# Kernel tuning notes

Measured on AMD Instinct MI355X. Metric: run time of the kernel, lower is better.

The kernel has to match this reference:

```python
import jax, jax.numpy as jnp
import numpy as np

N, A, C = 2048, 256, 100   # batch, feat_dim, num_classes
LAT = A // 2               # latent_dim = feat_dim // 2
BN_EPS = 1e-5


def setup_inputs() -> dict:
    key = jax.random.key(0)
    ks = jax.random.split(key, 8)
    s = jax.random.normal(ks[0], (N, A), dtype=jnp.float32)
    y = jax.random.randint(ks[1], (N,), 0, C)
    ratio = jnp.float32(0.5)
    W1 = jax.random.normal(ks[2], (LAT, A), dtype=jnp.float32) / np.sqrt(A)
    b1 = jnp.zeros((LAT,), jnp.float32)
    gamma = jnp.ones((LAT,), jnp.float32)
    beta = jnp.zeros((LAT,), jnp.float32)
    W2 = jax.random.normal(ks[3], (A, LAT), dtype=jnp.float32) / np.sqrt(LAT)
    b2 = jnp.zeros((A,), jnp.float32)
    Wfc = jax.random.normal(ks[4], (C, A), dtype=jnp.float32) / np.sqrt(A)
    bfc = jnp.zeros((C,), jnp.float32)
    # per-class covariance table [C, A, A], symmetric PSD like a real EstimatorCV state
    M = jax.random.normal(ks[5], (C, A, A), dtype=jnp.float32)
    cov = jnp.einsum('cab,cdb->cad', M, M) / A
    return {"s": s, "y": y, "ratio": ratio, "W1": W1, "b1": b1,
            "gamma": gamma, "beta": beta, "W2": W2, "b2": b2,
            "Wfc": Wfc, "bfc": bfc, "cov": cov}


def reference(s, y, ratio, W1, b1, gamma, beta, W2, b2, Wfc, bfc, cov):
    # pred: Linear -> BatchNorm1d (train-mode batch stats) -> ReLU -> Linear -> ReLU
    h = s @ W1.T + b1                                   # [N, LAT]
    mu = jnp.mean(h, axis=0)
    var = jnp.var(h, axis=0)                            # biased, as torch BN
    h = (h - mu) / jnp.sqrt(var + BN_EPS) * gamma + beta
    h = jax.nn.relu(h)
    f = jax.nn.relu(h @ W2.T + b2)                      # [N, A]
    z = f @ Wfc.T + bfc                                 # [N, C]

    # correct_z: diag of (W_i - W_y) cov[y] (W_i - W_y)^T, computed without the
    # wasted off-diagonal bmm of the original
    cov_sg = jax.lax.stop_gradient(cov)                 # cov is detached in source
    Wy = Wfc[y]                                         # [N, A]
    diff = Wfc[None, :, :] - Wy[:, None, :]             # [N, C, A]
    CVy = cov_sg[y]                                     # [N, A, A]
    tmp = jnp.einsum('nca,nab->ncb', diff, CVy)         # [N, C, A]
    sigma2 = jnp.sum(tmp * diff, axis=-1)               # [N, C] = diag of quad form
    return z + ratio * 0.5 * sigma2
```

## Files before the change

### kernel.cpp

```cpp
#include <hip/hip_runtime.h>

#define Nn  2048
#define Aa  256
#define Cc  100
#define LAT 128
#define BN_EPS 1e-5f

#define OFF_HB   0
#define OFF_SUMS (OFF_HB + Nn*LAT/2)
#define OFF_SP   (OFF_SUMS + 128*256)

typedef __attribute__((ext_vector_type(8))) short bf16x8;
typedef __attribute__((ext_vector_type(4))) float f32x4;

__device__ __forceinline__ short f2bf(float f) {
    unsigned u = __float_as_uint(f);
    u = (u + 0x7FFFu + ((u >> 16) & 1u)) >> 16;
    return (short)u;
}
__device__ __forceinline__ float bf2f(short h) {
    return __uint_as_float(((unsigned)(unsigned short)h) << 16);
}

#define DPITCH 264

__global__ __launch_bounds__(256) void kA(
    const float* __restrict__ s, const float* __restrict__ W1,
    const float* __restrict__ b1, const float* __restrict__ Wfc,
    const float* __restrict__ cov,
    short* __restrict__ hB, float* __restrict__ sums, float* __restrict__ Spart)
{
    __shared__ __align__(16) char smem[112 * DPITCH * 2 + 4 * 112 * 4];
    const int bid = blockIdx.x;
    const int t = threadIdx.x;
    const int w = t >> 6, l = t & 63, il = l & 15, q = l >> 4;

    if (bid < 200) {
        short* Dlds = (short*)smem;
        float (*red)[112] = (float(*)[112])(smem + 112 * DPITCH * 2);
        const int k  = bid >> 1;
        const int nh = bid & 1;
        const float* covk = cov + (size_t)k * (Aa * Aa);

        {
            const int c4 = t & 63;
            float4 wk = *(const float4*)&Wfc[(size_t)k * Aa + c4 * 4];
#pragma unroll
            for (int j = 0; j < 28; j++) {
                int row = (t >> 6) + j * 4;
                short4 o;
                if (row < Cc) {
                    float4 v = *(const float4*)&Wfc[(size_t)row * Aa + c4 * 4];
                    o.x = f2bf(v.x - wk.x); o.y = f2bf(v.y - wk.y);
                    o.z = f2bf(v.z - wk.z); o.w = f2bf(v.w - wk.w);
                } else {
                    o.x = 0; o.y = 0; o.z = 0; o.w = 0;
                }
                *(short4*)&Dlds[row * DPITCH + c4 * 4] = o;
            }
        }
        __syncthreads();

        const int bbase = nh * 128 + w * 32;

        f32x4 acc[7][2];
#pragma unroll
        for (int m = 0; m < 7; m++) {
            acc[m][0] = (f32x4){0.f,0.f,0.f,0.f};
            acc[m][1] = (f32x4){0.f,0.f,0.f,0.f};
        }

        const float* brow0 = covk + (size_t)(bbase + il) * Aa;
        const float* brow1 = covk + (size_t)(bbase + 16 + il) * Aa;

#pragma unroll
        for (int sgk = 0; sgk < 8; sgk++) {
            const int a0 = sgk * 32 + q * 8;
            bf16x8 bm0, bm1;
            {
                float4 u0 = *(const float4*)&brow0[a0];
                float4 u1 = *(const float4*)&brow0[a0 + 4];
                bm0[0]=f2bf(u0.x); bm0[1]=f2bf(u0.y); bm0[2]=f2bf(u0.z); bm0[3]=f2bf(u0.w);
                bm0[4]=f2bf(u1.x); bm0[5]=f2bf(u1.y); bm0[6]=f2bf(u1.z); bm0[7]=f2bf(u1.w);
                float4 v0 = *(const float4*)&brow1[a0];
                float4 v1 = *(const float4*)&brow1[a0 + 4];
                bm1[0]=f2bf(v0.x); bm1[1]=f2bf(v0.y); bm1[2]=f2bf(v0.z); bm1[3]=f2bf(v0.w);
                bm1[4]=f2bf(v1.x); bm1[5]=f2bf(v1.y); bm1[6]=f2bf(v1.z); bm1[7]=f2bf(v1.w);
            }
#pragma unroll
            for (int m = 0; m < 7; m++) {
                bf16x8 am = *(bf16x8*)&Dlds[(m * 16 + il) * DPITCH + a0];
                acc[m][0] = __builtin_amdgcn_mfma_f32_16x16x32_bf16(am, bm0, acc[m][0], 0, 0, 0);
                acc[m][1] = __builtin_amdgcn_mfma_f32_16x16x32_bf16(am, bm1, acc[m][1], 0, 0, 0);
            }
        }

#pragma unroll
        for (int m = 0; m < 7; m++) {
            float sacc[4] = {0.f, 0.f, 0.f, 0.f};
#pragma unroll
            for (int nf = 0; nf < 2; nf++) {
                int bcol = bbase + nf * 16 + il;
#pragma unroll
                for (int r = 0; r < 4; r++) {
                    int crow = m * 16 + q * 4 + r;
                    float dv = bf2f(Dlds[crow * DPITCH + bcol]);
                    sacc[r] = fmaf(dv, acc[m][nf][r], sacc[r]);
                }
            }
#pragma unroll
            for (int r = 0; r < 4; r++) {
                float v = sacc[r];
                v += __shfl_xor(v, 1);
                v += __shfl_xor(v, 2);
                v += __shfl_xor(v, 4);
                v += __shfl_xor(v, 8);
                if (il == 0) red[w][m * 16 + q * 4 + r] = v;
            }
        }
        __syncthreads();
        if (t < Cc)
            Spart[nh * (Cc * Cc) + k * Cc + t] =
                red[0][t] + red[1][t] + red[2][t] + red[3][t];
    } else {
        const int bid2 = bid - 200;
        const int row0 = bid2 * 16;
        const int colw = w * 32;

        f32x4 acc[2];
        acc[0] = (f32x4){0.f,0.f,0.f,0.f};
        acc[1] = (f32x4){0.f,0.f,0.f,0.f};

        const float* arow = s  + (size_t)(row0 + il) * Aa;
        const float* bp0  = W1 + (size_t)(colw + il) * Aa;
        const float* bp1  = W1 + (size_t)(colw + 16 + il) * Aa;

#pragma unroll
        for (int ks = 0; ks < 8; ks++) {
            const int k0 = ks * 32 + q * 8;
            float4 u0 = *(const float4*)&arow[k0];
            float4 u1 = *(const float4*)&arow[k0 + 4];
            bf16x8 am;
            am[0]=f2bf(u0.x); am[1]=f2bf(u0.y); am[2]=f2bf(u0.z); am[3]=f2bf(u0.w);
            am[4]=f2bf(u1.x); am[5]=f2bf(u1.y); am[6]=f2bf(u1.z); am[7]=f2bf(u1.w);
            float4 v0 = *(const float4*)&bp0[k0];
            float4 v1 = *(const float4*)&bp0[k0 + 4];
            bf16x8 bm0;
            bm0[0]=f2bf(v0.x); bm0[1]=f2bf(v0.y); bm0[2]=f2bf(v0.z); bm0[3]=f2bf(v0.w);
            bm0[4]=f2bf(v1.x); bm0[5]=f2bf(v1.y); bm0[6]=f2bf(v1.z); bm0[7]=f2bf(v1.w);
            float4 x0 = *(const float4*)&bp1[k0];
            float4 x1 = *(const float4*)&bp1[k0 + 4];
            bf16x8 bm1;
            bm1[0]=f2bf(x0.x); bm1[1]=f2bf(x0.y); bm1[2]=f2bf(x0.z); bm1[3]=f2bf(x0.w);
            bm1[4]=f2bf(x1.x); bm1[5]=f2bf(x1.y); bm1[6]=f2bf(x1.z); bm1[7]=f2bf(x1.w);
            acc[0] = __builtin_amdgcn_mfma_f32_16x16x32_bf16(am, bm0, acc[0], 0, 0, 0);
            acc[1] = __builtin_amdgcn_mfma_f32_16x16x32_bf16(am, bm1, acc[1], 0, 0, 0);
        }

#pragma unroll
        for (int n = 0; n < 2; n++) {
            const int col = colw + n * 16 + il;
            const float bias = b1[col];
            float s1 = 0.f, s2 = 0.f;
#pragma unroll
            for (int r = 0; r < 4; r++) {
                float v = acc[n][r] + bias;
                hB[(size_t)(row0 + q * 4 + r) * LAT + col] = f2bf(v);
                s1 += v; s2 += v * v;
            }
            s1 += __shfl_xor(s1, 16); s1 += __shfl_xor(s1, 32);
            s2 += __shfl_xor(s2, 16); s2 += __shfl_xor(s2, 32);
            if (q == 0) {
                sums[bid2 * 256 + col]       = s1;
                sums[bid2 * 256 + 128 + col] = s2;
            }
        }
    }
}

#define FPITCH 264

__global__ __launch_bounds__(256) void kB(
    const short* __restrict__ hB, const float* __restrict__ sums,
    const float* __restrict__ gamma, const float* __restrict__ beta,
    const float* __restrict__ W2, const float* __restrict__ b2,
    const float* __restrict__ Wfc, const float* __restrict__ bfc,
    const float* __restrict__ Spart, const int* __restrict__ y,
    const float* __restrict__ ratio, float* __restrict__ out)
{
    __shared__ float scL[LAT], shL[LAT];
    __shared__ short fLDS[16 * FPITCH];
    const int t = threadIdx.x;
    const int w = t >> 6, l = t & 63, il = l & 15, q = l >> 4;
    const int row0 = blockIdx.x * 16;

    if (t < 128) {
        float a1 = 0.f, a2 = 0.f;
#pragma unroll 8
        for (int b = 0; b < 128; b++) {
            a1 += sums[b * 256 + t];
            a2 += sums[b * 256 + 128 + t];
        }
        float mu  = a1 * (1.0f / Nn);
        float var = a2 * (1.0f / Nn) - mu * mu;
        float inv = rsqrtf(var + BN_EPS);
        float sc  = gamma[t] * inv;
        scL[t] = sc;
        shL[t] = beta[t] - mu * sc;
    }
    __syncthreads();

    f32x4 acc3[4];
#pragma unroll
    for (int n = 0; n < 4; n++) acc3[n] = (f32x4){0.f,0.f,0.f,0.f};

    const short* arow = hB + (size_t)(row0 + il) * LAT;
#pragma unroll
    for (int ks = 0; ks < 4; ks++) {
        const int k0 = ks * 32 + q * 8;
        bf16x8 ha = *(const bf16x8*)&arow[k0];
        bf16x8 am;
#pragma unroll
        for (int j = 0; j < 8; j++) {
            float fv = fmaf(bf2f(ha[j]), scL[k0 + j], shL[k0 + j]);
            am[j] = f2bf(fmaxf(fv, 0.f));
        }
#pragma unroll
        for (int n = 0; n < 4; n++) {
            const int col = w * 64 + n * 16 + il;
            float4 v0 = *(const float4*)&W2[(size_t)col * LAT + k0];
            float4 v1 = *(const float4*)&W2[(size_t)col * LAT + k0 + 4];
            bf16x8 bm;
            bm[0]=f2bf(v0.x); bm[1]=f2bf(v0.y); bm[2]=f2bf(v0.z); bm[3]=f2bf(v0.w);
            bm[4]=f2bf(v1.x); bm[5]=f2bf(v1.y); bm[6]=f2bf(v1.z); bm[7]=f2bf(v1.w);
            acc3[n] = __builtin_amdgcn_mfma_f32_16x16x32_bf16(am, bm, acc3[n], 0, 0, 0);
        }
    }
#pragma unroll
    for (int n = 0; n < 4; n++) {
        const int col = w * 64 + n * 16 + il;
        const float bias = b2[col];
#pragma unroll
        for (int r = 0; r < 4; r++) {
            float v = fmaxf(acc3[n][r] + bias, 0.f);
            fLDS[(q * 4 + r) * FPITCH + col] = f2bf(v);
        }
    }
    __syncthreads();

    f32x4 acc4[2];
    acc4[0] = (f32x4){0.f,0.f,0.f,0.f};
    acc4[1] = (f32x4){0.f,0.f,0.f,0.f};
#pragma unroll
    for (int ks = 0; ks < 8; ks++) {
        const int k0 = ks * 32 + q * 8;
        bf16x8 am = *(const bf16x8*)&fLDS[il * FPITCH + k0];
#pragma unroll
        for (int n = 0; n < 2; n++) {
            const int col = w * 32 + n * 16 + il;
            const int crow = col < Cc ? col : Cc - 1;
            float4 v0 = *(const float4*)&Wfc[(size_t)crow * Aa + k0];
            float4 v1 = *(const float4*)&Wfc[(size_t)crow * Aa + k0 + 4];
            bf16x8 bm;
            bm[0]=f2bf(v0.x); bm[1]=f2bf(v0.y); bm[2]=f2bf(v0.z); bm[3]=f2bf(v0.w);
            bm[4]=f2bf(v1.x); bm[5]=f2bf(v1.y); bm[6]=f2bf(v1.z); bm[7]=f2bf(v1.w);
            acc4[n] = __builtin_amdgcn_mfma_f32_16x16x32_bf16(am, bm, acc4[n], 0, 0, 0);
        }
    }

    const float coef = 0.5f * ratio[0];
    const int4 yv4 = *(const int4*)&y[row0 + q * 4];
    const int yr[4] = {yv4.x, yv4.y, yv4.z, yv4.w};

#pragma unroll
    for (int n = 0; n < 2; n++) {
        const int col = w * 32 + n * 16 + il;
        if (col < Cc) {
            const float bias = bfc[col];
#pragma unroll
            for (int r = 0; r < 4; r++) {
                float sp0 = Spart[yr[r] * Cc + col];
                float sp1 = Spart[Cc * Cc + yr[r] * Cc + col];
                out[(size_t)(row0 + q * 4 + r) * Cc + col] =
                    acc4[n][r] + bias + coef * (sp0 + sp1);
            }
        }
    }
}

extern "C" void kernel_launch(void* const* d_in, const int* in_sizes, int n_in,
                              void* d_out, int out_size, void* d_ws, size_t ws_size,
                              hipStream_t stream)
{
    const float* s     = (const float*)d_in[0];
    const int*   y     = (const int*)  d_in[1];
    const float* ratio = (const float*)d_in[2];
    const float* W1    = (const float*)d_in[3];
    const float* b1    = (const float*)d_in[4];
    const float* gamma = (const float*)d_in[5];
    const float* beta  = (const float*)d_in[6];
    const float* W2    = (const float*)d_in[7];
    const float* b2    = (const float*)d_in[8];
    const float* Wfc   = (const float*)d_in[9];
    const float* bfc   = (const float*)d_in[10];
    const float* cov   = (const float*)d_in[11];
    float* out = (float*)d_out;
    float* ws  = (float*)d_ws;

    short* hB    = (short*)(ws + OFF_HB);
    float* sums  = ws + OFF_SUMS;
    float* Spart = ws + OFF_SP;

    hipLaunchKernelGGL(kA, dim3(328), dim3(256), 0, stream,
                       s, W1, b1, Wfc, cov, hB, sums, Spart);
    hipLaunchKernelGGL(kB, dim3(128), dim3(256), 0, stream,
                       hB, sums, gamma, beta, W2, b2, Wfc, bfc, Spart, y, ratio, out);
}
```

Baseline: 38.79 us.

## Split covariance quad-form into quarter blocks and precast weights to bf16 in kA

The covariance quad-form work per class is now split across four blocks instead of two, giving 400 blocks with a single MFMA accumulator column per wave. This aims to raise parallelism and cut register pressure on the bandwidth-heavy cov read. Two extra blocks in kA pre-convert W2 and Wfc to bf16 in workspace, so kB loads bf16x8 directly instead of converting fp32 per block. The bf16 conversion now uses the HIP intrinsic. In exchange, the Dlds setup is duplicated across more blocks and kB reads four partial sums instead of two.

Result: faster. 35.24 us (-9.2%).

```diff
diff --git a/kernel.cpp b/kernel.cpp
--- a/kernel.cpp
+++ b/kernel.cpp
@@ -1,4 +1,5 @@
 #include <hip/hip_runtime.h>
+#include <hip/hip_bf16.h>
 
 #define Nn  2048
 #define Aa  256
@@ -9,14 +10,14 @@
 #define OFF_HB   0
 #define OFF_SUMS (OFF_HB + Nn*LAT/2)
 #define OFF_SP   (OFF_SUMS + 128*256)
+#define OFF_W2B  (OFF_SP + 4*Cc*Cc)
+#define OFF_WFB  (OFF_W2B + Aa*LAT/2)
 
 typedef __attribute__((ext_vector_type(8))) short bf16x8;
 typedef __attribute__((ext_vector_type(4))) float f32x4;
 
 __device__ __forceinline__ short f2bf(float f) {
-    unsigned u = __float_as_uint(f);
-    u = (u + 0x7FFFu + ((u >> 16) & 1u)) >> 16;
-    return (short)u;
+    return (short)__bfloat16_as_ushort(__float2bfloat16(f));
 }
 __device__ __forceinline__ float bf2f(short h) {
     return __uint_as_float(((unsigned)(unsigned short)h) << 16);
@@ -27,19 +28,20 @@
 __global__ __launch_bounds__(256) void kA(
     const float* __restrict__ s, const float* __restrict__ W1,
     const float* __restrict__ b1, const float* __restrict__ Wfc,
-    const float* __restrict__ cov,
-    short* __restrict__ hB, float* __restrict__ sums, float* __restrict__ Spart)
+    const float* __restrict__ W2, const float* __restrict__ cov,
+    short* __restrict__ hB, float* __restrict__ sums, float* __restrict__ Spart,
+    short* __restrict__ W2b, short* __restrict__ Wfcb)
 {
     __shared__ __align__(16) char smem[112 * DPITCH * 2 + 4 * 112 * 4];
     const int bid = blockIdx.x;
     const int t = threadIdx.x;
     const int w = t >> 6, l = t & 63, il = l & 15, q = l >> 4;
 
-    if (bid < 200) {
+    if (bid < 400) {
         short* Dlds = (short*)smem;
         float (*red)[112] = (float(*)[112])(smem + 112 * DPITCH * 2);
-        const int k  = bid >> 1;
-        const int nh = bid & 1;
+        const int k  = bid >> 2;
+        const int nq = bid & 3;
         const float* covk = cov + (size_t)k * (Aa * Aa);
 
         {
@@ -61,52 +63,37 @@
         }
         __syncthreads();
 
-        const int bbase = nh * 128 + w * 32;
-
-        f32x4 acc[7][2];
-#pragma unroll
-        for (int m = 0; m < 7; m++) {
-            acc[m][0] = (f32x4){0.f,0.f,0.f,0.f};
-            acc[m][1] = (f32x4){0.f,0.f,0.f,0.f};
-        }
-
-        const float* brow0 = covk + (size_t)(bbase + il) * Aa;
-        const float* brow1 = covk + (size_t)(bbase + 16 + il) * Aa;
+        const int bbase = nq * 64 + w * 16;
+
+        f32x4 acc[7];
+#pragma unroll
+        for (int m = 0; m < 7; m++) acc[m] = (f32x4){0.f,0.f,0.f,0.f};
+
+        const float* brow = covk + (size_t)(bbase + il) * Aa;
 
 #pragma unroll
         for (int sgk = 0; sgk < 8; sgk++) {
             const int a0 = sgk * 32 + q * 8;
-            bf16x8 bm0, bm1;
-            {
-                float4 u0 = *(const float4*)&brow0[a0];
-                float4 u1 = *(const float4*)&brow0[a0 + 4];
-                bm0[0]=f2bf(u0.x); bm0[1]=f2bf(u0.y); bm0[2]=f2bf(u0.z); bm0[3]=f2bf(u0.w);
-                bm0[4]=f2bf(u1.x); bm0[5]=f2bf(u1.y); bm0[6]=f2bf(u1.z); bm0[7]=f2bf(u1.w);
-                float4 v0 = *(const float4*)&brow1[a0];
-                float4 v1 = *(const float4*)&brow1[a0 + 4];
-                bm1[0]=f2bf(v0.x); bm1[1]=f2bf(v0.y); bm1[2]=f2bf(v0.z); bm1[3]=f2bf(v0.w);
-                bm1[4]=f2bf(v1.x); bm1[5]=f2bf(v1.y); bm1[6]=f2bf(v1.z); bm1[7]=f2bf(v1.w);
-            }
+            float4 u0 = *(const float4*)&brow[a0];
+            float4 u1 = *(const float4*)&brow[a0 + 4];
+            bf16x8 bm;
+            bm[0]=f2bf(u0.x); bm[1]=f2bf(u0.y); bm[2]=f2bf(u0.z); bm[3]=f2bf(u0.w);
+            bm[4]=f2bf(u1.x); bm[5]=f2bf(u1.y); bm[6]=f2bf(u1.z); bm[7]=f2bf(u1.w);
 #pragma unroll
             for (int m = 0; m < 7; m++) {
                 bf16x8 am = *(bf16x8*)&Dlds[(m * 16 + il) * DPITCH + a0];
-                acc[m][0] = __builtin_amdgcn_mfma_f32_16x16x32_bf16(am, bm0, acc[m][0], 0, 0, 0);
-                acc[m][1] = __builtin_amdgcn_mfma_f32_16x16x32_bf16(am, bm1, acc[m][1], 0, 0, 0);
+                acc[m] = __builtin_amdgcn_mfma_f32_16x16x32_bf16(am, bm, acc[m], 0, 0, 0);
             }
         }
 
 #pragma unroll
         for (int m = 0; m < 7; m++) {
-            float sacc[4] = {0.f, 0.f, 0.f, 0.f};
-#pragma unroll
-            for (int nf = 0; nf < 2; nf++) {
-                int bcol = bbase + nf * 16 + il;
-#pragma unroll
-                for (int r = 0; r < 4; r++) {
-                    int crow = m * 16 + q * 4 + r;
-                    float dv = bf2f(Dlds[crow * DPITCH + bcol]);
-                    sacc[r] = fmaf(dv, acc[m][nf][r], sacc[r]);
-                }
+            const int bcol = bbase + il;
+            float sacc[4];
+#pragma unroll
+            for (int r = 0; r < 4; r++) {
+                int crow = m * 16 + q * 4 + r;
+                sacc[r] = bf2f(Dlds[crow * DPITCH + bcol]) * acc[m][r];
             }
 #pragma unroll
             for (int r = 0; r < 4; r++) {
@@ -120,10 +107,10 @@
         }
         __syncthreads();
         if (t < Cc)
-            Spart[nh * (Cc * Cc) + k * Cc + t] =
+            Spart[nq * (Cc * Cc) + k * Cc + t] =
                 red[0][t] + red[1][t] + red[2][t] + red[3][t];
-    } else {
-        const int bid2 = bid - 200;
+    } else if (bid < 528) {
+        const int bid2 = bid - 400;
         const int row0 = bid2 * 16;
         const int colw = w * 32;
 
@@ -175,6 +162,22 @@
                 sums[bid2 * 256 + 128 + col] = s2;
             }
         }
+    } else if (bid == 528) {
+        for (int i = t * 4; i < Aa * LAT; i += 1024) {
+            float4 v = *(const float4*)&W2[i];
+            short4 o = {f2bf(v.x), f2bf(v.y), f2bf(v.z), f2bf(v.w)};
+            *(short4*)&W2b[i] = o;
+        }
+    } else {
+        for (int i = t * 4; i < 128 * Aa; i += 1024) {
+            int row = i >> 8;
+            short4 o = {0, 0, 0, 0};
+            if (row < Cc) {
+                float4 v = *(const float4*)&Wfc[i];
+                o.x = f2bf(v.x); o.y = f2bf(v.y); o.z = f2bf(v.z); o.w = f2bf(v.w);
+            }
+            *(short4*)&Wfcb[i] = o;
+        }
     }
 }
 
@@ -183,8 +186,8 @@
 __global__ __launch_bounds__(256) void kB(
     const short* __restrict__ hB, const float* __restrict__ sums,
     const float* __restrict__ gamma, const float* __restrict__ beta,
-    const float* __restrict__ W2, const float* __restrict__ b2,
-    const float* __restrict__ Wfc, const float* __restrict__ bfc,
+    const short* __restrict__ W2b, const float* __restrict__ b2,
+    const short* __restrict__ Wfcb, const float* __restrict__ bfc,
     const float* __restrict__ Spart, const int* __restrict__ y,
     const float* __restrict__ ratio, float* __restrict__ out)
 {
@@ -228,11 +231,7 @@
 #pragma unroll
         for (int n = 0; n < 4; n++) {
             const int col = w * 64 + n * 16 + il;
-            float4 v0 = *(const float4*)&W2[(size_t)col * LAT + k0];
-            float4 v1 = *(const float4*)&W2[(size_t)col * LAT + k0 + 4];
-            bf16x8 bm;
-            bm[0]=f2bf(v0.x); bm[1]=f2bf(v0.y); bm[2]=f2bf(v0.z); bm[3]=f2bf(v0.w);
-            bm[4]=f2bf(v1.x); bm[5]=f2bf(v1.y); bm[6]=f2bf(v1.z); bm[7]=f2bf(v1.w);
+            bf16x8 bm = *(const bf16x8*)&W2b[(size_t)col * LAT + k0];
             acc3[n] = __builtin_amdgcn_mfma_f32_16x16x32_bf16(am, bm, acc3[n], 0, 0, 0);
         }
     }
@@ -258,12 +257,7 @@
 #pragma unroll
         for (int n = 0; n < 2; n++) {
             const int col = w * 32 + n * 16 + il;
-            const int crow = col < Cc ? col : Cc - 1;
-            float4 v0 = *(const float4*)&Wfc[(size_t)crow * Aa + k0];
-            float4 v1 = *(const float4*)&Wfc[(size_t)crow * Aa + k0 + 4];
-            bf16x8 bm;
-            bm[0]=f2bf(v0.x); bm[1]=f2bf(v0.y); bm[2]=f2bf(v0.z); bm[3]=f2bf(v0.w);
-            bm[4]=f2bf(v1.x); bm[5]=f2bf(v1.y); bm[6]=f2bf(v1.z); bm[7]=f2bf(v1.w);
+            bf16x8 bm = *(const bf16x8*)&Wfcb[(size_t)col * Aa + k0];
             acc4[n] = __builtin_amdgcn_mfma_f32_16x16x32_bf16(am, bm, acc4[n], 0, 0, 0);
         }
     }
@@ -279,10 +273,10 @@
             const float bias = bfc[col];
 #pragma unroll
             for (int r = 0; r < 4; r++) {
-                float sp0 = Spart[yr[r] * Cc + col];
-                float sp1 = Spart[Cc * Cc + yr[r] * Cc + col];
+                const float* sp = &Spart[yr[r] * Cc + col];
+                float sv = sp[0] + sp[Cc*Cc] + sp[2*Cc*Cc] + sp[3*Cc*Cc];
                 out[(size_t)(row0 + q * 4 + r) * Cc + col] =
-                    acc4[n][r] + bias + coef * (sp0 + sp1);
+                    acc4[n][r] + bias + coef * sv;
             }
         }
     }
@@ -310,9 +304,11 @@
     short* hB    = (short*)(ws + OFF_HB);
     float* sums  = ws + OFF_SUMS;
     float* Spart = ws + OFF_SP;
-
-    hipLaunchKernelGGL(kA, dim3(328), dim3(256), 0, stream,
-                       s, W1, b1, Wfc, cov, hB, sums, Spart);
+    short* W2b   = (short*)(ws + OFF_W2B);
+    short* Wfcb  = (short*)(ws + OFF_WFB);
+
+    hipLaunchKernelGGL(kA, dim3(530), dim3(256), 0, stream,
+                       s, W1, b1, Wfc, W2, cov, hB, sums, Spart, W2b, Wfcb);
     hipLaunchKernelGGL(kB, dim3(128), dim3(256), 0, stream,
-                       hB, sums, gamma, beta, W2, b2, Wfc, bfc, Spart, y, ratio, out);
-}
+                       hB, sums, gamma, beta, W2b, b2, Wfcb, bfc, Spart, y, ratio, out);
+}
```
